# Performance work log

Hardware: AMD Instinct MI355X
Metric: run time of the kernel (lower is better)

Reference implementation:

```python
import jax, jax.numpy as jnp
import numpy as np

# ---- config (from init_kwargs) ----
PRE_NMS_THRESH = 0.05
K = 200                    # pre_nms_top_n (fixed-size top-k for jit)
NUM_CLASSES = 80
FPN_STRIDE = 8
MASK_SCALE_FACTOR = 2
MASK_STRIDE = FPN_STRIDE / MASK_SCALE_FACTOR  # 4.0
IMG_H, IMG_W = 768, 768


def setup_inputs() -> dict:
    key = jax.random.key(0)
    ks = jax.random.split(key, 6)
    N, C, H, W, DIM = 2, NUM_CLASSES, 96, 96, 32
    # FCOS-style locations for the stride-8 level: center of each cell
    ys, xs = jnp.meshgrid(jnp.arange(H, dtype=jnp.float32),
                          jnp.arange(W, dtype=jnp.float32), indexing='ij')
    locations = jnp.stack([xs.reshape(-1), ys.reshape(-1)], axis=1) * FPN_STRIDE + FPN_STRIDE // 2
    return {
        'locations': locations,                                                 # [HW, 2]
        'box_cls': jax.random.normal(ks[0], (N, C, H, W), jnp.float32) - 2.0,   # mostly below thresh
        'box_regression': jax.random.uniform(ks[1], (N, 4, H, W), jnp.float32) * 100.0,
        'centerness': jax.random.normal(ks[2], (N, 1, H, W), jnp.float32),
        'proposal_embed': jax.random.normal(ks[3], (N, DIM, H, W), jnp.float32),
        'proposal_margin': jax.random.uniform(ks[4], (N, 1, H, W), jnp.float32, minval=0.1, maxval=2.0),
        'pixel_embed': jax.random.normal(ks[5], (N, DIM, 192, 192), jnp.float32),
    }


def reference(locations, box_cls, box_regression, centerness,
              proposal_embed, proposal_margin, pixel_embed):
    N, C, H, W = box_cls.shape
    DIM = proposal_embed.shape[1]
    o_h = pixel_embed.shape[2] * MASK_SCALE_FACTOR
    o_w = pixel_embed.shape[3] * MASK_SCALE_FACTOR

    # interpolate(pixel_embed, size=(o_h, o_w), mode='bilinear', align_corners=False)
    pix_up = jax.image.resize(pixel_embed, (N, DIM, o_h, o_w), method='bilinear')

    # NCHW -> [N, HW, C] flattening (matches permute(0,2,3,1).reshape)
    scores = jax.nn.sigmoid(jnp.transpose(box_cls.reshape(N, C, H * W), (0, 2, 1)))   # [N, HW, C]
    ctr = jax.nn.sigmoid(centerness.reshape(N, H * W))                                # [N, HW]
    reg = jnp.transpose(box_regression.reshape(N, 4, H * W), (0, 2, 1))               # [N, HW, 4]
    emb = jnp.transpose(proposal_embed.reshape(N, DIM, H * W), (0, 2, 1))             # [N, HW, DIM]
    mar = proposal_margin.reshape(N, H * W)                                           # [N, HW]

    xs = jnp.arange(o_w, dtype=jnp.float32)
    ys = jnp.arange(o_h, dtype=jnp.float32)

    def per_image(s, c, r, e, m, pix):
        # threshold + centerness-weighted score; invalid candidates rank last
        cand = s > PRE_NMS_THRESH                       # [HW, C]
        sc = s * c[:, None]                             # [HW, C]
        flat = jnp.where(cand, sc, -1.0).reshape(-1)    # [HW*C]
        topv, topi = jax.lax.top_k(flat, K)             # fixed-size top-k
        loc_idx = topi // C                             # [K]
        labels = topi % C + 1                           # [K]
        valid = topv > 0.0                              # padded slots when < K candidates

        # box decode: [x - l, y - t, x + r, y + b], clipped to image
        loc = locations[loc_idx]                        # [K, 2]
        rr = r[loc_idx]                                 # [K, 4]
        x1 = jnp.clip(loc[:, 0] - rr[:, 0], 0.0, IMG_W - 1)
        y1 = jnp.clip(loc[:, 1] - rr[:, 1], 0.0, IMG_H - 1)
        x2 = jnp.clip(loc[:, 0] + rr[:, 2], 0.0, IMG_W - 1)
        y2 = jnp.clip(loc[:, 1] + rr[:, 3], 0.0, IMG_H - 1)
        boxes = jnp.stack([x1, y1, x2, y2], axis=1)     # [K, 4]

        # boxes_to_masks at mask stride: binary inside-box masks [K, o_h, o_w]
        mb = boxes / MASK_STRIDE
        in_x = (xs[None, :] >= mb[:, 0:1]) & (xs[None, :] <= mb[:, 2:3])  # [K, o_w]
        in_y = (ys[None, :] >= mb[:, 1:2]) & (ys[None, :] <= mb[:, 3:4])  # [K, o_h]
        box_mask = in_y[:, :, None] & in_x[:, None, :]

        # pixel-embed distance mask: exp(-||pix - e_k||^2 * margin_k)
        ek = e[loc_idx]                                 # [K, DIM]
        mk = m[loc_idx]                                 # [K]
        p = pix.reshape(DIM, o_h * o_w)                 # [DIM, P]
        d2 = (jnp.sum(ek * ek, axis=1)[:, None]
              + jnp.sum(p * p, axis=0)[None, :]
              - 2.0 * ek @ p)                           # [K, P] via GEMM
        prob = jnp.exp(-d2 * mk[:, None]).reshape(K, o_h, o_w)
        masks = prob * box_mask.astype(prob.dtype) * valid[:, None, None].astype(prob.dtype)
        return masks

    masks = jax.vmap(per_image)(scores, ctr, reg, emb, mar, pix_up)  # [N, K, o_h, o_w]
    return masks
```

## Files before the change

### kernel.cpp

```cpp
#include <hip/hip_runtime.h>
#include <cmath>


namespace {
constexpr int NIMG = 2;
constexpr int NC   = 80;
constexpr int NHW  = 96 * 96;
constexpr int NCHW = NC * NHW;
constexpr int NDIM = 32;
constexpr int PH = 192, PW = 192;
constexpr int OH = 384, OW = 384;
constexpr int KTOP = 200;
constexpr int CAP = 4096;
constexpr int MCAP = 1024;
constexpr int LCAP = 512;
constexpr float PRE_THRESH = 0.05f;
constexpr unsigned KEY_ZERO = 0x80000000u;
constexpr float IMG_MAX = 767.0f;

constexpr int NBOX = NIMG * KTOP;
constexpr int ZTILES = 6;
constexpr int NZB = NBOX * ZTILES;

constexpr int NF4 = NCHW / 4;
constexpr int SEL_BLOCKS = 128;
constexpr int SEL_STRIDE = SEL_BLOCKS * 256;
constexpr int SEL_ITERS = (NF4 + SEL_STRIDE - 1) / SEL_STRIDE;

constexpr int WS_HIST1  = 0;
constexpr int WS_CNT    = WS_HIST1 + NIMG * 2048;
constexpr int WS_BAR    = WS_CNT + NIMG;
constexpr int WS_TICK   = WS_BAR + 1;
constexpr int WS_ZERO_WORDS = WS_TICK + NIMG;
constexpr int WS_PAIRS  = 4104;
constexpr int WS_PARAMS = WS_PAIRS + NIMG * CAP * 2;
constexpr int PARAM_WORDS = 40;

typedef float f4 __attribute__((ext_vector_type(4)));
}

__device__ __forceinline__ unsigned key_of(float f) {
  unsigned u = __float_as_uint(f);
  return (u & 0x80000000u) ? ~u : (u | 0x80000000u);
}

__global__ __launch_bounds__(256) void k_zero_ws(unsigned* __restrict__ ws) {
  for (int j = threadIdx.x; j < WS_ZERO_WORDS; j += 256) ws[j] = 0u;
}

__global__ __launch_bounds__(256) void k_select(
    const float* __restrict__ box_cls, const float* __restrict__ ctrness,
    const float* __restrict__ locations, const float* __restrict__ box_reg,
    const float* __restrict__ pemb, const float* __restrict__ pmar,
    unsigned* __restrict__ ws) {
  __shared__ unsigned hist[2048];
  __shared__ unsigned sh_sum[256];
  __shared__ int sh_bk[2];
  __shared__ unsigned loc[LCAP][2];
  __shared__ int lcnt;
  __shared__ unsigned gbase;
  __shared__ int sh_last;
  const int t = threadIdx.x;
  const int n = blockIdx.x >= SEL_BLOCKS;
  const int bi = blockIdx.x - n * SEL_BLOCKS;

  for (int i = t; i < 2048; i += 256) hist[i] = 0;
  __syncthreads();
  const float* cls = box_cls + n * NCHW;
  const float* ctr = ctrness + n * NHW;
  unsigned kk[SEL_ITERS][4];
  #pragma unroll
  for (int s = 0; s < SEL_ITERS; ++s) {
    const int j4 = s * SEL_STRIDE + bi * 256 + t;
    if (j4 < NF4) {
      const int j = j4 * 4;
      const int c = j / NHW;
      const int hw = j - c * NHW;
      const f4 xv = *reinterpret_cast<const f4*>(cls + j);
      const f4 cv = *reinterpret_cast<const f4*>(ctr + hw);
      #pragma unroll
      for (int q = 0; q < 4; ++q) {
        const float sg = 1.0f / (1.0f + expf(-xv[q]));
        float v = -1.0f;
        if (sg > PRE_THRESH) v = sg * (1.0f / (1.0f + expf(-cv[q])));
        const unsigned k = key_of(v);
        kk[s][q] = k;
        if (k > KEY_ZERO) atomicAdd(&hist[k >> 21], 1u);
      }
    } else {
      #pragma unroll
      for (int q = 0; q < 4; ++q) kk[s][q] = 0u;
    }
  }
  __syncthreads();
  {
    unsigned* gh = ws + WS_HIST1 + n * 2048;
    for (int i = t; i < 2048; i += 256) { unsigned v = hist[i]; if (v) atomicAdd(&gh[i], v); }
  }

  __syncthreads();
  if (t == 0) {
    atomicAdd(ws + WS_BAR, 1u);
    while (__hip_atomic_load(ws + WS_BAR, __ATOMIC_RELAXED,
                             __HIP_MEMORY_SCOPE_AGENT) < (unsigned)(2 * SEL_BLOCKS)) {
      __builtin_amdgcn_s_sleep(2);
    }
  }
  __syncthreads();

  if (t == 0) { sh_bk[0] = -1; sh_bk[1] = KTOP; }
  {
    const unsigned* gh = ws + WS_HIST1 + n * 2048;
    unsigned local = 0;
    for (int j = 0; j < 8; ++j) { unsigned v = gh[t * 8 + j]; hist[t * 8 + j] = v; local += v; }
    sh_sum[t] = local;
  }
  __syncthreads();
  {
    unsigned S = 0;
    for (int j = t + 1; j < 256; ++j) S += sh_sum[j];
    int cand_b = -1;
    unsigned cand_above = 0;
    unsigned run = S;
    for (int j = 7; j >= 0; --j) {
      const unsigned cv = hist[t * 8 + j];
      if (cand_b < 0 && run + cv >= (unsigned)KTOP) { cand_b = t * 8 + j; cand_above = run; }
      run += cv;
    }
    if (cand_b >= 0) atomicMax(&sh_bk[0], cand_b);
    __syncthreads();
    if (cand_b >= 0 && cand_b == sh_bk[0]) sh_bk[1] = KTOP - (int)cand_above;
    __syncthreads();
  }
  const unsigned b1 = (unsigned)(sh_bk[0] < 0 ? 0 : sh_bk[0]);
  int krem = sh_bk[1];

  if (t == 0) lcnt = 0;
  __syncthreads();
  #pragma unroll
  for (int s = 0; s < SEL_ITERS; ++s) {
    #pragma unroll
    for (int q = 0; q < 4; ++q) {
      const unsigned k = kk[s][q];
      if ((k >> 21) < b1) continue;
      const int j = (s * SEL_STRIDE + bi * 256 + t) * 4 + q;
      const int c = j / NHW;
      const int hw = j - c * NHW;
      const int p = atomicAdd(&lcnt, 1);
      if (p < LCAP) { loc[p][0] = k; loc[p][1] = (unsigned)(hw * NC + c); }
    }
  }
  __syncthreads();
  const int lc = min(lcnt, LCAP);
  if (t == 0) gbase = atomicAdd(ws + WS_CNT + n, (unsigned)lc);
  __syncthreads();
  for (int i = t; i < lc; i += 256) {
    const unsigned pos = gbase + (unsigned)i;
    if (pos < (unsigned)CAP) {
      __hip_atomic_store(&ws[WS_PAIRS + (n * CAP + (int)pos) * 2], loc[i][0],
                         __ATOMIC_RELAXED, __HIP_MEMORY_SCOPE_AGENT);
      __hip_atomic_store(&ws[WS_PAIRS + (n * CAP + (int)pos) * 2 + 1], loc[i][1],
                         __ATOMIC_RELAXED, __HIP_MEMORY_SCOPE_AGENT);
    }
  }

  __syncthreads();
  if (t == 0) {
    const unsigned old = atomicAdd(ws + WS_TICK + n, 1u);
    sh_last = (old == (unsigned)(SEL_BLOCKS - 1)) ? 1 : 0;
  }
  __syncthreads();
  if (!sh_last) return;

  __shared__ uint2 P[CAP];
  __shared__ unsigned h256[256];
  __shared__ unsigned mKey[MCAP], mRef[MCAP];
  __shared__ int sh_b, sh_t;
  for (int s = t; s < KTOP; s += 256) ws[WS_PARAMS + (n * KTOP + s) * PARAM_WORDS] = 0u;
  const int cnt = min((int)__hip_atomic_load(ws + WS_CNT + n, __ATOMIC_RELAXED,
                                             __HIP_MEMORY_SCOPE_AGENT), CAP);
  for (int i = t; i < cnt; i += 256) {
    P[i].x = __hip_atomic_load(&ws[WS_PAIRS + (n * CAP + i) * 2],
                               __ATOMIC_RELAXED, __HIP_MEMORY_SCOPE_AGENT);
    P[i].y = __hip_atomic_load(&ws[WS_PAIRS + (n * CAP + i) * 2 + 1],
                               __ATOMIC_RELAXED, __HIP_MEMORY_SCOPE_AGENT);
  }
  __syncthreads();

  unsigned prefix = b1;
  int shift = 21;
  #pragma unroll
  for (int level = 0; level < 2; ++level) {
    const int newshift = shift - 8;
    h256[t] = 0;
    if (t == 0) sh_b = 0;
    __syncthreads();
    for (int i = t; i < cnt; i += 256) {
      const unsigned k = P[i].x;
      if ((k >> shift) == prefix) atomicAdd(&h256[(k >> newshift) & 255u], 1u);
    }
    __syncthreads();
    const unsigned hv = h256[t];
    unsigned S = 0;
    for (int j = t + 1; j < 256; ++j) S += h256[j];
    if (S + hv >= (unsigned)krem) atomicMax(&sh_b, t);
    __syncthreads();
    const int b = sh_b;
    if (t == b) sh_t = krem - (int)S;
    __syncthreads();
    krem = sh_t;
    prefix = (prefix << 8) | (unsigned)b;
    shift = newshift;
    __syncthreads();
  }

  if (t == 0) sh_t = 0;
  __syncthreads();
  for (int i = t; i < cnt; i += 256) {
    const unsigned k = P[i].x;
    if ((k >> 5) >= prefix) {
      const int pos = atomicAdd(&sh_t, 1);
      if (pos < MCAP) { mKey[pos] = k; mRef[pos] = P[i].y; }
    }
  }
  __syncthreads();
  const int m = min(sh_t, MCAP);

  for (int i = t; i < m; i += 256) {
    const unsigned ki = mKey[i], ri = mRef[i];
    int rank = 0;
    for (int j = 0; j < m; ++j) {
      const unsigned kj = mKey[j], rj = mRef[j];
      rank += (kj > ki || (kj == ki && rj < ri)) ? 1 : 0;
    }
    if (rank >= KTOP) continue;
    unsigned* pp = ws + WS_PARAMS + (n * KTOP + rank) * PARAM_WORDS;
    int valid = 0;
    if (ki > KEY_ZERO) {
      const int hw = (int)ri / NC;
      const float lx = locations[2 * hw], ly = locations[2 * hw + 1];
      const float rl = box_reg[(n * 4 + 0) * NHW + hw];
      const float rt = box_reg[(n * 4 + 1) * NHW + hw];
      const float rr = box_reg[(n * 4 + 2) * NHW + hw];
      const float rb = box_reg[(n * 4 + 3) * NHW + hw];
      const float x1 = fminf(fmaxf(lx - rl, 0.f), IMG_MAX);
      const float y1 = fminf(fmaxf(ly - rt, 0.f), IMG_MAX);
      const float x2 = fminf(fmaxf(lx + rr, 0.f), IMG_MAX);
      const float y2 = fminf(fmaxf(ly + rb, 0.f), IMG_MAX);
      const int ix0 = max(0, (int)ceilf(x1 * 0.25f));
      const int ix1 = min(OW - 1, (int)floorf(x2 * 0.25f));
      const int iy0 = max(0, (int)ceilf(y1 * 0.25f));
      const int iy1 = min(OH - 1, (int)floorf(y2 * 0.25f));
      if (ix0 <= ix1 && iy0 <= iy1) {
        valid = 1;
        pp[1] = (unsigned)ix0; pp[2] = (unsigned)ix1;
        pp[3] = (unsigned)iy0; pp[4] = (unsigned)iy1;
        reinterpret_cast<float*>(pp)[5] = pmar[n * NHW + hw];
        float* ep = reinterpret_cast<float*>(pp) + 8;
        #pragma unroll
        for (int d = 0; d < NDIM; ++d) ep[d] = pemb[(n * NDIM + d) * NHW + hw];
      }
    }
    pp[0] = (unsigned)valid;
  }
}

__global__ __launch_bounds__(256) void k_out(const float* __restrict__ pix,
                                             const unsigned* __restrict__ ws,
                                             float* __restrict__ out) {
  const int bid = blockIdx.x;
  const int t = threadIdx.x;
  if (bid >= NBOX) {
    const int zb = bid - NBOX;
    const int nk = zb / ZTILES;
    const int rt = zb - nk * ZTILES;
    const int y0 = rt * 64;
    const unsigned* meta = ws + WS_PARAMS + nk * PARAM_WORDS;
    f4* ob4 = reinterpret_cast<f4*>(out + (size_t)nk * (OH * OW)) + y0 * (OW / 4);
    const f4 z = {0.f, 0.f, 0.f, 0.f};
    int qa = 0, qb = -1, iy0 = 0, iy1 = -1;
    bool overlap = false;
    if (meta[0]) {
      iy0 = (int)meta[3]; iy1 = (int)meta[4];
      if (iy1 >= y0 && iy0 < y0 + 64) {
        overlap = true;
        qa = (int)meta[1] >> 2;
        qb = (int)meta[2] >> 2;
      }
    }
    if (!overlap) {
      #pragma unroll
      for (int i = 0; i < 24; ++i) ob4[i * 256 + t] = z;
    } else {
      for (int i = 0; i < 24; ++i) {
        const int idx = i * 256 + t;
        const int y = y0 + idx / 96;
        const int q = idx - (idx / 96) * 96;
        if (y >= iy0 && y <= iy1 && q >= qa && q <= qb) continue;
        ob4[idx] = z;
      }
    }
    return;
  }

  const int nk = bid;
  const unsigned* meta = ws + WS_PARAMS + nk * PARAM_WORDS;
  if (meta[0] == 0u) return;
  const int ix0 = (int)meta[1], ix1 = (int)meta[2];
  const int iy0 = (int)meta[3], iy1 = (int)meta[4];
  const int xp0 = (ix0 >> 2) << 2;
  const int xp1 = (ix1 >> 2) * 4 + 3;
  const float margin = __uint_as_float(meta[5]);
  float e[NDIM];
  {
    const float4* e4 = reinterpret_cast<const float4*>(meta + 8);
    #pragma unroll
    for (int q = 0; q < NDIM / 4; ++q) {
      const float4 v = e4[q];
      e[4 * q + 0] = v.x; e[4 * q + 1] = v.y; e[4 * q + 2] = v.z; e[4 * q + 3] = v.w;
    }
  }
  const int n = nk / KTOP;
  const float* peb = pix + (size_t)n * NDIM * PH * PW;
  float* ob = out + (size_t)nk * (OH * OW);

  const int tx = t & 63;
  const int ts = t >> 6;
  const int h = iy1 - iy0 + 1;
  const int shh = (h + 3) >> 2;
  const int ybeg = iy0 + ts * shh;
  const int yend = min(iy0 + (ts + 1) * shh, iy1 + 1);

  for (int c = xp0 + tx; c <= xp1; c += 64) {
    const bool inx = (c >= ix0) && (c <= ix1);
    const float sx = 0.5f * (float)c - 0.25f;
    const float xf = floorf(sx);
    const float fx = sx - xf;
    const int xs0 = max((int)xf, 0);
    const int xs1 = min((int)xf + 1, PW - 1);
    float qa_[NDIM], qb_[NDIM];
    int ra = -9, rb = -9;
    for (int y = ybeg; y < yend; ++y) {
      float val = 0.f;
      if (inx) {
        const float sy = 0.5f * (float)y - 0.25f;
        const float yf = floorf(sy);
        const float fy = sy - yf;
        const int ys0 = max((int)yf, 0);
        const int ys1 = min((int)yf + 1, PH - 1);
        if (ys0 != ra) {
          if (ys0 == rb) {
            #pragma unroll
            for (int d = 0; d < NDIM; ++d) qa_[d] = qb_[d];
          } else {
            const float* p = peb + (size_t)ys0 * PW;
            #pragma unroll
            for (int d = 0; d < NDIM; ++d)
              qa_[d] = (1.f - fx) * p[d * PH * PW + xs0] + fx * p[d * PH * PW + xs1];
          }
          ra = ys0;
        }
        if (ys1 != rb) {
          if (ys1 == ra) {
            #pragma unroll
            for (int d = 0; d < NDIM; ++d) qb_[d] = qa_[d];
          } else {
            const float* p = peb + (size_t)ys1 * PW;
            #pragma unroll
            for (int d = 0; d < NDIM; ++d)
              qb_[d] = (1.f - fx) * p[d * PH * PW + xs0] + fx * p[d * PH * PW + xs1];
          }
          rb = ys1;
        }
        float d2 = 0.f;
        #pragma unroll
        for (int d = 0; d < NDIM; ++d) {
          const float pv = qa_[d] + fy * (qb_[d] - qa_[d]);
          const float df = e[d] - pv;
          d2 = fmaf(df, df, d2);
        }
        val = expf(-d2 * margin);
      }
      ob[(size_t)y * OW + c] = val;
    }
  }
}

extern "C" void kernel_launch(void* const* d_in, const int* in_sizes, int n_in,
                              void* d_out, int out_size, void* d_ws, size_t ws_size,
                              hipStream_t stream) {
  const float* locations = (const float*)d_in[0];
  const float* box_cls   = (const float*)d_in[1];
  const float* box_reg   = (const float*)d_in[2];
  const float* ctrness   = (const float*)d_in[3];
  const float* pemb      = (const float*)d_in[4];
  const float* pmar      = (const float*)d_in[5];
  const float* pix       = (const float*)d_in[6];
  float* out = (float*)d_out;
  unsigned* ws = (unsigned*)d_ws;

  k_zero_ws<<<dim3(1), dim3(256), 0, stream>>>(ws);
  k_select <<<dim3(2 * SEL_BLOCKS), dim3(256), 0, stream>>>(
      box_cls, ctrness, locations, box_reg, pemb, pmar, ws);
  k_out    <<<dim3(NBOX + NZB), dim3(256), 0, stream>>>(pix, ws, out);
}
```

Measured before the change: 100.8 us.

## Overlap full output zero-fill with top-k selection and restrict box kernel to box

Extra blocks are appended to the selection kernel that zero the entire output while the histogram and top-k selection run. The box kernel then only writes pixels inside each valid box, dropping the per-tile overlap tests and in-x predicate. The intent is to hide the large zero-store traffic behind the latency-bound selection phase. In exchange, pixels inside boxes are now written twice, and the zero blocks share the GPU with the spin-barrier selection blocks.

```diff
diff --git a/kernel.cpp b/kernel.cpp
--- a/kernel.cpp
+++ b/kernel.cpp
@@ -24,6 +24,7 @@
 
 constexpr int NF4 = NCHW / 4;
 constexpr int SEL_BLOCKS = 128;
+constexpr int NSEL = 2 * SEL_BLOCKS;
 constexpr int SEL_STRIDE = SEL_BLOCKS * 256;
 constexpr int SEL_ITERS = (NF4 + SEL_STRIDE - 1) / SEL_STRIDE;
 
@@ -48,11 +49,21 @@
   for (int j = threadIdx.x; j < WS_ZERO_WORDS; j += 256) ws[j] = 0u;
 }
 
-__global__ __launch_bounds__(256) void k_select(
+__global__ __launch_bounds__(256) void k_main(
     const float* __restrict__ box_cls, const float* __restrict__ ctrness,
     const float* __restrict__ locations, const float* __restrict__ box_reg,
     const float* __restrict__ pemb, const float* __restrict__ pmar,
-    unsigned* __restrict__ ws) {
+    unsigned* __restrict__ ws, float* __restrict__ out) {
+  const int t = threadIdx.x;
+  if (blockIdx.x >= NSEL) {
+    const int zb = blockIdx.x - NSEL;
+    f4* ob4 = reinterpret_cast<f4*>(out) + (size_t)zb * (64 * OW / 4);
+    const f4 z = {0.f, 0.f, 0.f, 0.f};
+    #pragma unroll
+    for (int i = 0; i < 24; ++i) ob4[i * 256 + t] = z;
+    return;
+  }
+
   __shared__ unsigned hist[2048];
   __shared__ unsigned sh_sum[256];
   __shared__ int sh_bk[2];
@@ -60,7 +71,6 @@
   __shared__ int lcnt;
   __shared__ unsigned gbase;
   __shared__ int sh_last;
-  const int t = threadIdx.x;
   const int n = blockIdx.x >= SEL_BLOCKS;
   const int bi = blockIdx.x - n * SEL_BLOCKS;
 
@@ -102,7 +112,7 @@
   if (t == 0) {
     atomicAdd(ws + WS_BAR, 1u);
     while (__hip_atomic_load(ws + WS_BAR, __ATOMIC_RELAXED,
-                             __HIP_MEMORY_SCOPE_AGENT) < (unsigned)(2 * SEL_BLOCKS)) {
+                             __HIP_MEMORY_SCOPE_AGENT) < (unsigned)NSEL) {
       __builtin_amdgcn_s_sleep(2);
     }
   }
@@ -265,51 +275,15 @@
   }
 }
 
-__global__ __launch_bounds__(256) void k_out(const float* __restrict__ pix,
+__global__ __launch_bounds__(256) void k_box(const float* __restrict__ pix,
                                              const unsigned* __restrict__ ws,
                                              float* __restrict__ out) {
-  const int bid = blockIdx.x;
+  const int nk = blockIdx.x;
   const int t = threadIdx.x;
-  if (bid >= NBOX) {
-    const int zb = bid - NBOX;
-    const int nk = zb / ZTILES;
-    const int rt = zb - nk * ZTILES;
-    const int y0 = rt * 64;
-    const unsigned* meta = ws + WS_PARAMS + nk * PARAM_WORDS;
-    f4* ob4 = reinterpret_cast<f4*>(out + (size_t)nk * (OH * OW)) + y0 * (OW / 4);
-    const f4 z = {0.f, 0.f, 0.f, 0.f};
-    int qa = 0, qb = -1, iy0 = 0, iy1 = -1;
-    bool overlap = false;
-    if (meta[0]) {
-      iy0 = (int)meta[3]; iy1 = (int)meta[4];
-      if (iy1 >= y0 && iy0 < y0 + 64) {
-        overlap = true;
-        qa = (int)meta[1] >> 2;
-        qb = (int)meta[2] >> 2;
-      }
-    }
-    if (!overlap) {
-      #pragma unroll
-      for (int i = 0; i < 24; ++i) ob4[i * 256 + t] = z;
-    } else {
-      for (int i = 0; i < 24; ++i) {
-        const int idx = i * 256 + t;
-        const int y = y0 + idx / 96;
-        const int q = idx - (idx / 96) * 96;
-        if (y >= iy0 && y <= iy1 && q >= qa && q <= qb) continue;
-        ob4[idx] = z;
-      }
-    }
-    return;
-  }
-
-  const int nk = bid;
   const unsigned* meta = ws + WS_PARAMS + nk * PARAM_WORDS;
   if (meta[0] == 0u) return;
   const int ix0 = (int)meta[1], ix1 = (int)meta[2];
   const int iy0 = (int)meta[3], iy1 = (int)meta[4];
-  const int xp0 = (ix0 >> 2) << 2;
-  const int xp1 = (ix1 >> 2) * 4 + 3;
   const float margin = __uint_as_float(meta[5]);
   float e[NDIM];
   {
@@ -331,8 +305,7 @@
   const int ybeg = iy0 + ts * shh;
   const int yend = min(iy0 + (ts + 1) * shh, iy1 + 1);
 
-  for (int c = xp0 + tx; c <= xp1; c += 64) {
-    const bool inx = (c >= ix0) && (c <= ix1);
+  for (int c = ix0 + tx; c <= ix1; c += 64) {
     const float sx = 0.5f * (float)c - 0.25f;
     const float xf = floorf(sx);
     const float fx = sx - xf;
@@ -341,47 +314,43 @@
     float qa_[NDIM], qb_[NDIM];
     int ra = -9, rb = -9;
     for (int y = ybeg; y < yend; ++y) {
-      float val = 0.f;
-      if (inx) {
-        const float sy = 0.5f * (float)y - 0.25f;
-        const float yf = floorf(sy);
-        const float fy = sy - yf;
-        const int ys0 = max((int)yf, 0);
-        const int ys1 = min((int)yf + 1, PH - 1);
-        if (ys0 != ra) {
-          if (ys0 == rb) {
-            #pragma unroll
-            for (int d = 0; d < NDIM; ++d) qa_[d] = qb_[d];
-          } else {
-            const float* p = peb + (size_t)ys0 * PW;
-            #pragma unroll
-            for (int d = 0; d < NDIM; ++d)
-              qa_[d] = (1.f - fx) * p[d * PH * PW + xs0] + fx * p[d * PH * PW + xs1];
-          }
-          ra = ys0;
+      const float sy = 0.5f * (float)y - 0.25f;
+      const float yf = floorf(sy);
+      const float fy = sy - yf;
+      const int ys0 = max((int)yf, 0);
+      const int ys1 = min((int)yf + 1, PH - 1);
+      if (ys0 != ra) {
+        if (ys0 == rb) {
+          #pragma unroll
+          for (int d = 0; d < NDIM; ++d) qa_[d] = qb_[d];
+        } else {
+          const float* p = peb + (size_t)ys0 * PW;
+          #pragma unroll
+          for (int d = 0; d < NDIM; ++d)
+            qa_[d] = (1.f - fx) * p[d * PH * PW + xs0] + fx * p[d * PH * PW + xs1];
         }
-        if (ys1 != rb) {
-          if (ys1 == ra) {
-            #pragma unroll
-            for (int d = 0; d < NDIM; ++d) qb_[d] = qa_[d];
-          } else {
-            const float* p = peb + (size_t)ys1 * PW;
-            #pragma unroll
-            for (int d = 0; d < NDIM; ++d)
-              qb_[d] = (1.f - fx) * p[d * PH * PW + xs0] + fx * p[d * PH * PW + xs1];
-          }
-          rb = ys1;
+        ra = ys0;
+      }
+      if (ys1 != rb) {
+        if (ys1 == ra) {
+          #pragma unroll
+          for (int d = 0; d < NDIM; ++d) qb_[d] = qa_[d];
+        } else {
+          const float* p = peb + (size_t)ys1 * PW;
+          #pragma unroll
+          for (int d = 0; d < NDIM; ++d)
+            qb_[d] = (1.f - fx) * p[d * PH * PW + xs0] + fx * p[d * PH * PW + xs1];
         }
-        float d2 = 0.f;
-        #pragma unroll
-        for (int d = 0; d < NDIM; ++d) {
-          const float pv = qa_[d] + fy * (qb_[d] - qa_[d]);
-          const float df = e[d] - pv;
-          d2 = fmaf(df, df, d2);
-        }
-        val = expf(-d2 * margin);
-      }
-      ob[(size_t)y * OW + c] = val;
+        rb = ys1;
+      }
+      float d2 = 0.f;
+      #pragma unroll
+      for (int d = 0; d < NDIM; ++d) {
+        const float pv = qa_[d] + fy * (qb_[d] - qa_[d]);
+        const float df = e[d] - pv;
+        d2 = fmaf(df, df, d2);
+      }
+      ob[(size_t)y * OW + c] = expf(-d2 * margin);
     }
   }
 }
@@ -400,7 +369,7 @@
   unsigned* ws = (unsigned*)d_ws;
 
   k_zero_ws<<<dim3(1), dim3(256), 0, stream>>>(ws);
-  k_select <<<dim3(2 * SEL_BLOCKS), dim3(256), 0, stream>>>(
-      box_cls, ctrness, locations, box_reg, pemb, pmar, ws);
-  k_out    <<<dim3(NBOX + NZB), dim3(256), 0, stream>>>(pix, ws, out);
-}
+  k_main  <<<dim3(NSEL + NZB), dim3(256), 0, stream>>>(
+      box_cls, ctrness, locations, box_reg, pemb, pmar, ws, out);
+  k_box   <<<dim3(NBOX), dim3(256), 0, stream>>>(pix, ws, out);
+}
```

Result: slower. 104.9 us (+4.1%).
